# Kernel tuning notes

Measured on AMD Instinct MI355X. Metric: run time of the kernel, lower is better.

Reference implementation:

```python
import jax, jax.numpy as jnp
import numpy as np

ROPE_BASE = 10000.0

def apply_rope(x, offset=0):
    # x: [B, H, L, Dh], traditional (interleaved-pair) RoPE
    B, H, L, Dh = x.shape
    pos = jnp.arange(L, dtype=jnp.float32) + offset            # [L]
    freqs = ROPE_BASE ** (-jnp.arange(0, Dh, 2, dtype=jnp.float32) / Dh)  # [Dh/2]
    theta = pos[:, None] * freqs[None, :]                      # [L, Dh/2]
    cos, sin = jnp.cos(theta), jnp.sin(theta)
    x1 = x[..., 0::2]                                          # [B,H,L,Dh/2]
    x2 = x[..., 1::2]
    r1 = x1 * cos - x2 * sin
    r2 = x1 * sin + x2 * cos
    return jnp.stack([r1, r2], axis=-1).reshape(B, H, L, Dh)


def setup_inputs() -> dict:
    key = jax.random.key(0)
    ks = jax.random.split(key, 5)
    B, L, D = 2, 2048, 2048
    s = 1.0 / np.sqrt(D)
    x = jax.random.normal(ks[0], (B, L, D), dtype=jnp.float32)
    # additive causal mask (0 on/below diagonal, -1e9 above)
    mask = jnp.where(jnp.tril(jnp.ones((L, L), dtype=bool)), 0.0, -1e9).astype(jnp.float32)
    Wq = jax.random.normal(ks[1], (D, D), dtype=jnp.float32) * s
    Wk = jax.random.normal(ks[2], (D, D), dtype=jnp.float32) * s
    Wv = jax.random.normal(ks[3], (D, D), dtype=jnp.float32) * s
    Wo = jax.random.normal(ks[4], (D, D), dtype=jnp.float32) * s
    return {"x": x, "mask": mask, "Wq": Wq, "Wk": Wk, "Wv": Wv, "Wo": Wo}


def reference(x, mask, Wq, Wk, Wv, Wo):
    num_heads = 16
    B, L, D = x.shape
    Dh = D // num_heads
    q = (x @ Wq.T).reshape(B, L, num_heads, Dh).transpose(0, 2, 1, 3)  # [B,H,L,Dh]
    k = (x @ Wk.T).reshape(B, L, num_heads, Dh).transpose(0, 2, 1, 3)
    v = (x @ Wv.T).reshape(B, L, num_heads, Dh).transpose(0, 2, 1, 3)
    q = apply_rope(q)
    k = apply_rope(k)
    scale = 1.0 / jnp.sqrt(jnp.float32(Dh))
    scores = jnp.einsum('bhqd,bhkd->bhqk', q * scale, k) + mask  # [B,H,L,L]
    probs = jax.nn.softmax(scores, axis=-1)
    vh = jnp.einsum('bhqk,bhkd->bhqd', probs, v)                 # [B,H,L,Dh]
    vh = vh.transpose(0, 2, 1, 3).reshape(B, L, D)
    out = vh @ Wo.T
    return out, k, v
```

## Files before the change

kernel.cpp:

```cpp
#include <hip/hip_runtime.h>

typedef __attribute__((ext_vector_type(4))) float f32x4;
typedef __attribute__((ext_vector_type(8))) __bf16 bf16x8;

__device__ __forceinline__ unsigned short f2b(float f) {
  unsigned int u = __builtin_bit_cast(unsigned int, f);
  u = (u + 0x7fffu + ((u >> 16) & 1u)) >> 16;
  return (unsigned short)u;
}
__device__ __forceinline__ float b2f(unsigned short h) {
  unsigned int u = ((unsigned int)h) << 16;
  return __builtin_bit_cast(float, u);
}
__device__ __forceinline__ void gl_lds16(const void* g, void* l) {
  __builtin_amdgcn_global_load_lds(
      (const __attribute__((address_space(1))) void*)g,
      (__attribute__((address_space(3))) void*)l, 16, 0, 0);
}

__global__ void cast_kernel(const float* __restrict__ src,
                            unsigned short* __restrict__ dst, int n4) {
  int i = blockIdx.x * blockDim.x + threadIdx.x;
  if (i >= n4) return;
  float4 v = ((const float4*)src)[i];
  ushort4 o;
  o.x = f2b(v.x); o.y = f2b(v.y); o.z = f2b(v.z); o.w = f2b(v.w);
  ((ushort4*)dst)[i] = o;
}

__global__ void cast4_kernel(const float* __restrict__ s0, const float* __restrict__ s1,
                             const float* __restrict__ s2, const float* __restrict__ s3,
                             unsigned short* __restrict__ d0, unsigned short* __restrict__ d1,
                             unsigned short* __restrict__ d2, unsigned short* __restrict__ d3,
                             int n4) {
  int i = blockIdx.x * blockDim.x + threadIdx.x;
  if (i >= n4) return;
  const float* src = blockIdx.y == 0 ? s0 : blockIdx.y == 1 ? s1 : blockIdx.y == 2 ? s2 : s3;
  unsigned short* dst = blockIdx.y == 0 ? d0 : blockIdx.y == 1 ? d1 : blockIdx.y == 2 ? d2 : d3;
  float4 v = ((const float4*)src)[i];
  ushort4 o;
  o.x = f2b(v.x); o.y = f2b(v.y); o.z = f2b(v.z); o.w = f2b(v.w);
  ((ushort4*)dst)[i] = o;
}

__global__ void rope_table_kernel(float2* __restrict__ tab) {
  int idx = blockIdx.x * blockDim.x + threadIdx.x;
  int l = idx >> 6, i = idx & 63;
  float freq = __builtin_amdgcn_exp2f(-(float)(2 * i) * (13.287712379549449f / 128.0f));
  float th = (float)l * freq;
  tab[idx] = make_float2(cosf(th), sinf(th));
}

__global__ void rope_apply_kernel(unsigned short* __restrict__ qb,
                                  unsigned short* __restrict__ kb,
                                  float* __restrict__ kout,
                                  const float2* __restrict__ tab) {
  const float QS = 0.12751743f;
  int z = blockIdx.y;
  int p = blockIdx.x * blockDim.x + threadIdx.x;
  int i = p & 63;
  int t = p >> 6;
  int h = t & 15; t >>= 4;
  int l = t & 2047;
  int b = t >> 11;
  int base = ((b * 2048 + l) * 2048) + h * 128 + 2 * i;
  unsigned short* buf = z ? kb : qb;
  float x1 = b2f(buf[base]), x2 = b2f(buf[base + 1]);
  float2 cs = tab[l * 64 + i];
  float r1 = x1 * cs.x - x2 * cs.y;
  float r2 = x1 * cs.y + x2 * cs.x;
  if (z == 1) {
    buf[base] = f2b(r1);
    buf[base + 1] = f2b(r2);
    int obase = ((b * 16 + h) * 2048 + l) * 128 + 2 * i;
    kout[obase] = r1; kout[obase + 1] = r2;
  } else {
    buf[base] = f2b(r1 * QS);
    buf[base + 1] = f2b(r2 * QS);
  }
}

__global__ __launch_bounds__(256) void transpose_v_kernel(const unsigned short* __restrict__ vb,
                                                          unsigned short* __restrict__ vt,
                                                          float* __restrict__ vout) {
  __shared__ unsigned short t[32][33];
  int bz = blockIdx.z;
  int b = bz >> 4, h = bz & 15;
  int l0 = blockIdx.x * 32, d0 = blockIdx.y * 32;
  const unsigned short* src = vb + (size_t)b * 2048 * 2048 + h * 128;
  unsigned short* dst = vt + (size_t)bz * 128 * 2048;
  int tx = threadIdx.x & 31, ty = threadIdx.x >> 5;
#pragma unroll
  for (int i = 0; i < 4; ++i) {
    unsigned short u = src[(size_t)(l0 + ty + 8 * i) * 2048 + d0 + tx];
    t[ty + 8 * i][tx] = u;
    vout[((size_t)bz * 2048 + l0 + ty + 8 * i) * 128 + d0 + tx] = b2f(u);
  }
  __syncthreads();
#pragma unroll
  for (int i = 0; i < 4; ++i)
    dst[(size_t)(d0 + ty + 8 * i) * 2048 + l0 + tx] = t[tx][ty + 8 * i];
}

template <int BM, int NBN, int OUT_F32>
__global__ __launch_bounds__(512, 2) void gemm4(const unsigned short* __restrict__ A,
                                                const unsigned short* __restrict__ W,
                                                void* __restrict__ C) {
  constexpr int K = 2048, NT = 32;
  constexpr int AH = BM / 2;
  constexpr int MF = BM / 64;
  constexpr int AQ = AH / 64;
  __shared__ unsigned short Asm[2][2][AH * 64];
  __shared__ unsigned short Bsm[2][2][128 * 64];

  const int tid = threadIdx.x, lane = tid & 63, wv = tid >> 6;
  const int wr = wv >> 2, wc = wv & 3;
  const int ln = lane & 15, kg = lane >> 4;

  const int cpx = (int)gridDim.x >> 3;
  const int swzb = ((int)blockIdx.x & 7) * cpx + ((int)blockIdx.x >> 3);
  const int bm = swzb / NBN, bn = swzb % NBN;
  const int m0 = bm * BM, n0 = bn * 256;

  const int rr = lane >> 3;
  const int sws = ((lane & 7) ^ (rr & 7)) * 8;
  const unsigned short* pA = A + (size_t)(m0 + wv * 8 * AQ + rr) * K + sws;
  const unsigned short* pB = W + (size_t)(n0 + wv * 16 + rr) * K + sws;

#define STA_(dd, hh, tt)                                                         \
  { _Pragma("unroll") for (int q = 0; q < AQ; ++q)                               \
      gl_lds16(pA + ((size_t)(hh)*AH + q * 8) * K + (size_t)(tt)*64,             \
               &Asm[dd][hh][(wv * 8 * AQ + q * 8) * 64 + lane * 8]); }
#define STB_(dd, hh, tt)                                                         \
  { _Pragma("unroll") for (int q = 0; q < 2; ++q)                                \
      gl_lds16(pB + ((size_t)(hh)*128 + q * 8) * K + (size_t)(tt)*64,            \
               &Bsm[dd][hh][(wv * 16 + q * 8) * 64 + lane * 8]); }

  const int sw0 = (kg ^ (ln & 7)) * 8;
  const int sw1 = ((4 + kg) ^ (ln & 7)) * 8;
  const int rae = (wr * (AH / 2) + ln) * 64;
  const int rbe = (wc * 32 + ln) * 64;

  f32x4 acc[2 * MF][4] = {};
  bf16x8 aA[MF][2], bB[2][2][2];

#define LDA_(dd, mh)                                                              \
  { _Pragma("unroll") for (int mf = 0; mf < MF; ++mf) {                           \
      aA[mf][0] = *(const bf16x8*)&Asm[dd][mh][rae + mf * 1024 + sw0];            \
      aA[mf][1] = *(const bf16x8*)&Asm[dd][mh][rae + mf * 1024 + sw1];            \
    } }
#define LDB_(dd, bh)                                                              \
  { _Pragma("unroll") for (int nf = 0; nf < 2; ++nf) {                            \
      bB[bh][nf][0] = *(const bf16x8*)&Bsm[dd][bh][rbe + nf * 1024 + sw0];        \
      bB[bh][nf][1] = *(const bf16x8*)&Bsm[dd][bh][rbe + nf * 1024 + sw1];        \
    } }

#define QMM(mh, bh)                                                               \
  {                                                                               \
    __builtin_amdgcn_s_setprio(1);                                                \
    _Pragma("unroll") for (int mf = 0; mf < MF; ++mf)                             \
        _Pragma("unroll") for (int nf = 0; nf < 2; ++nf) {                        \
      acc[(mh)*MF + mf][(bh)*2 + nf] = __builtin_amdgcn_mfma_f32_16x16x32_bf16(   \
          aA[mf][0], bB[bh][nf][0], acc[(mh)*MF + mf][(bh)*2 + nf], 0, 0, 0);     \
      acc[(mh)*MF + mf][(bh)*2 + nf] = __builtin_amdgcn_mfma_f32_16x16x32_bf16(   \
          aA[mf][1], bB[bh][nf][1], acc[(mh)*MF + mf][(bh)*2 + nf], 0, 0, 0);     \
    }                                                                             \
    __builtin_amdgcn_s_setprio(0);                                                \
  }

#define BAR   { __builtin_amdgcn_s_barrier(); __builtin_amdgcn_sched_barrier(0); }
#define VWAIT                                                                     \
  { if (BM == 256) { asm volatile("s_waitcnt vmcnt(4)" ::: "memory"); }           \
    else { asm volatile("s_waitcnt vmcnt(3)" ::: "memory"); } }
#define VW0   { asm volatile("s_waitcnt vmcnt(0)" ::: "memory"); }

  STA_(0, 0, 0); STB_(0, 0, 0); STB_(0, 1, 0); STA_(0, 1, 0);
  STA_(1, 0, 1); STB_(1, 1, 1);
  VWAIT;

  for (int T = 0; T < NT; T += 2) {
    const bool more = (T + 2) < NT;
    LDA_(0, 0); LDB_(0, 0);
    STB_(1, 0, T + 1);
    BAR; QMM(0, 0); BAR;
    LDB_(0, 1);
    STA_(1, 1, T + 1);
    BAR; QMM(0, 1); BAR;
    LDA_(0, 1);
    if (more) STA_(0, 0, T + 2);
    BAR; QMM(1, 1); BAR;
    if (more) { STB_(0, 1, T + 2); VWAIT; } else { VW0; }
    BAR; QMM(1, 0); BAR;
    LDA_(1, 0); LDB_(1, 0);
    if (more) STB_(0, 0, T + 2);
    BAR; QMM(0, 0); BAR;
    LDB_(1, 1);
    if (more) STA_(0, 1, T + 2);
    BAR; QMM(0, 1); BAR;
    LDA_(1, 1);
    if (more) STA_(1, 0, T + 3);
    BAR; QMM(1, 1); BAR;
    if (more) { STB_(1, 1, T + 3); VWAIT; }
    BAR; QMM(1, 0); BAR;
  }

  const int mat = bn >> 3;
  unsigned short* Cb = (unsigned short*)C;
  float* Cf = (float*)C;
#pragma unroll
  for (int mh = 0; mh < 2; ++mh)
#pragma unroll
    for (int mf = 0; mf < MF; ++mf)
#pragma unroll
      for (int j = 0; j < 4; ++j) {
        int row = m0 + mh * AH + wr * (AH / 2) + mf * 16 + kg * 4 + j;
        size_t rb = (size_t)mat * 8388608 + (size_t)row * 2048 + (size_t)((bn & 7) * 256);
#pragma unroll
        for (int bh = 0; bh < 2; ++bh)
#pragma unroll
          for (int nf = 0; nf < 2; ++nf) {
            int col = bh * 128 + wc * 32 + nf * 16 + ln;
            float v = acc[mh * MF + mf][bh * 2 + nf][j];
            if (OUT_F32) Cf[rb + col] = v;
            else Cb[rb + col] = f2b(v);
          }
      }
#undef STA_
#undef STB_
#undef LDA_
#undef LDB_
#undef QMM
#undef BAR
#undef VWAIT
#undef VW0
}

__global__ __launch_bounds__(256, 2) void attn5_kernel(const unsigned short* __restrict__ Qb,
                                                       const unsigned short* __restrict__ Kb,
                                                       const unsigned short* __restrict__ Vt,
                                                       unsigned short* __restrict__ Ob) {
  __shared__ unsigned short KS[2][8192];
  __shared__ unsigned short VS[8192];
  __shared__ unsigned short PS[4][2048];
  const int D = 2048, L = 2048;
  int tid = threadIdx.x, lane = tid & 63, w = tid >> 6;
  int ln = lane & 15, kg = lane >> 4;
  int bid = blockIdx.x;
  int g = bid >> 5, bh = bid & 31;
  int qt = (g < 8) ? (15 - g) : (g - 8);
  int b = bh >> 4, h = bh & 15;
  const size_t base = (size_t)b * L * D + h * 128;
  const unsigned short* Kp = Kb + base;
  const unsigned short* Qp = Qb + base;
  unsigned short* Op = Ob + base;
  const unsigned short* Vp = Vt + (size_t)bh * 128 * L;

  int q0 = qt * 128;
  int qw0 = q0 + w * 32;

  bf16x8 aq[2][4];
#pragma unroll
  for (int m = 0; m < 2; ++m)
#pragma unroll
    for (int kc = 0; kc < 4; ++kc)
      aq[m][kc] = *(const bf16x8*)&Qp[(size_t)(qw0 + m * 16 + ln) * D + kc * 32 + kg * 8];

  f32x4 o[2][8] = {};
  float m2[2][4], ls[2][4];
#pragma unroll
  for (int m = 0; m < 2; ++m)
#pragma unroll
    for (int j = 0; j < 4; ++j) { m2[m][j] = -1e30f; ls[m][j] = 0.f; }

  int l16 = lane >> 4, l8 = lane >> 3, l7 = lane & 7;

#define STAGE_K(T, NB)                                                                 \
  { int kv0_ = (T) << 6;                                                               \
    _Pragma("unroll") for (int i = 0; i < 4; ++i) {                                    \
      int cK = w * 4 + i;                                                              \
      int r = cK * 4 + l16;                                                            \
      int sw = ln ^ (r & 7);                                                           \
      gl_lds16(Kp + (size_t)(kv0_ + r) * D + sw * 8, &KS[NB][cK * 512 + lane * 8]); } }
#define STAGE_V(T)                                                                     \
  { int kv0_ = (T) << 6;                                                               \
    _Pragma("unroll") for (int i = 0; i < 4; ++i) {                                    \
      int cK = w * 4 + i;                                                              \
      int dh = cK * 8 + l8;                                                            \
      int sv = l7 ^ (dh & 7);                                                          \
      gl_lds16(Vp + (size_t)dh * L + kv0_ + sv * 8, &VS[cK * 512 + lane * 8]); } }

  int nt = 2 * qt + 2;
  int mask_t = 2 * qt + (w >> 1);

  STAGE_K(0, 0);
  __syncthreads();

  for (int t = 0; t < nt; ++t) {
    int cur = t & 1;
    STAGE_V(t);
    bool morek = (t + 1) < nt;
    if (morek) STAGE_K(t + 1, cur ^ 1);

    if (t <= mask_t) {
      int kv0 = t << 6;
      f32x4 s[2][4] = {};
#pragma unroll
      for (int n = 0; n < 4; ++n)
#pragma unroll
        for (int kc = 0; kc < 4; ++kc) {
          bf16x8 bk = *(const bf16x8*)&KS[cur][(n * 16 + ln) * 128 + (((kc << 2) + kg) ^ (ln & 7)) * 8];
          s[0][n] = __builtin_amdgcn_mfma_f32_16x16x32_bf16(aq[0][kc], bk, s[0][n], 0, 0, 0);
          s[1][n] = __builtin_amdgcn_mfma_f32_16x16x32_bf16(aq[1][kc], bk, s[1][n], 0, 0, 0);
        }
      if (t == mask_t) {
#pragma unroll
        for (int m = 0; m < 2; ++m)
#pragma unroll
          for (int n = 0; n < 4; ++n)
#pragma unroll
            for (int j = 0; j < 4; ++j)
              if (kv0 + n * 16 + ln > qw0 + m * 16 + kg * 4 + j) s[m][n][j] = -1e30f;
      }
      float pmax[2][4];
      bool near = true;
#pragma unroll
      for (int m = 0; m < 2; ++m)
#pragma unroll
        for (int j = 0; j < 4; ++j) {
          pmax[m][j] = fmaxf(fmaxf(s[m][0][j], s[m][1][j]), fmaxf(s[m][2][j], s[m][3][j]));
          near = near && (pmax[m][j] <= m2[m][j] + 8.0f);
        }
      if (!__all(near)) {
#pragma unroll
        for (int m = 0; m < 2; ++m)
#pragma unroll
          for (int j = 0; j < 4; ++j) {
            float mx = pmax[m][j];
#pragma unroll
            for (int d = 1; d < 16; d <<= 1) mx = fmaxf(mx, __shfl_xor(mx, d));
            mx = fmaxf(mx, m2[m][j]);
            float al = __builtin_amdgcn_exp2f(m2[m][j] - mx);
            m2[m][j] = mx;
            ls[m][j] *= al;
#pragma unroll
            for (int dt = 0; dt < 8; ++dt) o[m][dt][j] *= al;
          }
      }
#pragma unroll
      for (int m = 0; m < 2; ++m)
#pragma unroll
        for (int j = 0; j < 4; ++j) {
          int row = m * 16 + kg * 4 + j;
          float acc = 0.f;
#pragma unroll
          for (int n = 0; n < 4; ++n) {
            float p = __builtin_amdgcn_exp2f(s[m][n][j] - m2[m][j]);
            acc += p;
            unsigned int u = __builtin_bit_cast(unsigned int, p);
            PS[w][row * 64 + (((n * 2 + (ln >> 3)) ^ (row & 7)) * 8) + (ln & 7)] =
                (unsigned short)(u >> 16);
          }
          ls[m][j] += acc;
        }
    }

    if (morek) { asm volatile("s_waitcnt vmcnt(4)" ::: "memory"); }
    else       { asm volatile("s_waitcnt vmcnt(0)" ::: "memory"); }
    __builtin_amdgcn_s_barrier();
    __builtin_amdgcn_sched_barrier(0);

    if (t <= mask_t) {
      int kv0 = t << 6;
      (void)kv0;
#pragma unroll
      for (int kst = 0; kst < 2; ++kst) {
        bf16x8 ap0 = *(const bf16x8*)&PS[w][(ln) * 64 + (((kst << 2) + kg) ^ (ln & 7)) * 8];
        bf16x8 ap1 = *(const bf16x8*)&PS[w][(16 + ln) * 64 + (((kst << 2) + kg) ^ (ln & 7)) * 8];
#pragma unroll
        for (int dt = 0; dt < 8; ++dt) {
          bf16x8 bv = *(const bf16x8*)&VS[(dt * 16 + ln) * 64 + (((kst << 2) + kg) ^ (ln & 7)) * 8];
          o[0][dt] = __builtin_amdgcn_mfma_f32_16x16x32_bf16(ap0, bv, o[0][dt], 0, 0, 0);
          o[1][dt] = __builtin_amdgcn_mfma_f32_16x16x32_bf16(ap1, bv, o[1][dt], 0, 0, 0);
        }
      }
    }
    __syncthreads();
  }
#undef STAGE_K
#undef STAGE_V

#pragma unroll
  for (int m = 0; m < 2; ++m)
#pragma unroll
    for (int j = 0; j < 4; ++j) {
      float tsum = ls[m][j];
#pragma unroll
      for (int d = 1; d < 16; d <<= 1) tsum += __shfl_xor(tsum, d);
      float inv = 1.0f / tsum;
      int row = qw0 + m * 16 + kg * 4 + j;
#pragma unroll
      for (int dt = 0; dt < 8; ++dt)
        Op[(size_t)row * D + dt * 16 + ln] = f2b(o[m][dt][j] * inv);
    }
}

extern "C" void kernel_launch(void* const* d_in, const int* in_sizes, int n_in,
                              void* d_out, int out_size, void* d_ws, size_t ws_size,
                              hipStream_t stream) {
  const float* x  = (const float*)d_in[0];
  const float* Wq = (const float*)d_in[2];
  const float* Wk = (const float*)d_in[3];
  const float* Wv = (const float*)d_in[4];
  const float* Wo = (const float*)d_in[5];

  char* ws = (char*)d_ws;
  unsigned short* xb  = (unsigned short*)(ws + 0);
  unsigned short* wqb = (unsigned short*)(ws + 16777216);
  unsigned short* wkb = (unsigned short*)(ws + 25165824);
  unsigned short* wvb = (unsigned short*)(ws + 33554432);
  unsigned short* wob = (unsigned short*)(ws + 41943040);
  unsigned short* qb  = (unsigned short*)(ws + 50331648);
  unsigned short* kb  = (unsigned short*)(ws + 67108864);
  unsigned short* vb  = (unsigned short*)(ws + 83886080);
  float2* tab         = (float2*)(ws + 100663296);
  unsigned short* vt  = wqb;
  unsigned short* ob  = xb;

  float* out  = (float*)d_out;
  float* kout = out + 8388608;
  float* vout = out + 16777216;

  cast_kernel<<<8192, 256, 0, stream>>>(x, xb, 2097152);
  cast4_kernel<<<dim3(4096, 4), 256, 0, stream>>>(Wq, Wk, Wv, Wo, wqb, wkb, wvb, wob, 1048576);
  rope_table_kernel<<<512, 256, 0, stream>>>(tab);

  gemm4<256, 24, 0><<<384, 512, 0, stream>>>(xb, wqb, qb);

  transpose_v_kernel<<<dim3(64, 4, 32), 256, 0, stream>>>(vb, vt, vout);

  rope_apply_kernel<<<dim3(16384, 2), 256, 0, stream>>>(qb, kb, kout, tab);

  attn5_kernel<<<512, 256, 0, stream>>>(qb, kb, vt, ob);

  gemm4<128, 8, 1><<<256, 512, 0, stream>>>(ob, wob, out);
}
```

Before: 296.4 us.

## Merge prep and post-projection kernels, add MFMA priority hints in attention

The three cast/rope-table kernels are folded into one launch with a blockIdx.y selector, and the V transpose and RoPE apply kernels are folded into a second launch. This removes launch overhead and the gaps between small kernels. The attention kernel also raises wave priority with s_setprio around the MFMA loops so matrix work is issued ahead of other waves. The merged grids leave many idle blocks that exit early, and the transpose branch adds LDS use to the RoPE path, which may affect occupancy.

```diff
diff --git a/kernel.cpp b/kernel.cpp
--- a/kernel.cpp
+++ b/kernel.cpp
@@ -18,9 +18,28 @@
       (__attribute__((address_space(3))) void*)l, 16, 0, 0);
 }
 
-__global__ void cast_kernel(const float* __restrict__ src,
-                            unsigned short* __restrict__ dst, int n4) {
+__global__ void prep_kernel(const float* __restrict__ x, unsigned short* __restrict__ xb,
+                            const float* __restrict__ s0, const float* __restrict__ s1,
+                            const float* __restrict__ s2, const float* __restrict__ s3,
+                            unsigned short* __restrict__ d0, unsigned short* __restrict__ d1,
+                            unsigned short* __restrict__ d2, unsigned short* __restrict__ d3,
+                            float2* __restrict__ tab) {
+  int z = blockIdx.y;
   int i = blockIdx.x * blockDim.x + threadIdx.x;
+  if (z == 5) {
+    if (i >= 131072) return;
+    int l = i >> 6, k = i & 63;
+    float freq = __builtin_amdgcn_exp2f(-(float)(2 * k) * (13.287712379549449f / 128.0f));
+    float th = (float)l * freq;
+    tab[i] = make_float2(cosf(th), sinf(th));
+    return;
+  }
+  const float* src; unsigned short* dst; int n4;
+  if (z == 0)      { src = x;  dst = xb; n4 = 2097152; }
+  else if (z == 1) { src = s0; dst = d0; n4 = 1048576; }
+  else if (z == 2) { src = s1; dst = d1; n4 = 1048576; }
+  else if (z == 3) { src = s2; dst = d2; n4 = 1048576; }
+  else             { src = s3; dst = d3; n4 = 1048576; }
   if (i >= n4) return;
   float4 v = ((const float4*)src)[i];
   ushort4 o;
@@ -28,41 +47,43 @@
   ((ushort4*)dst)[i] = o;
 }
 
-__global__ void cast4_kernel(const float* __restrict__ s0, const float* __restrict__ s1,
-                             const float* __restrict__ s2, const float* __restrict__ s3,
-                             unsigned short* __restrict__ d0, unsigned short* __restrict__ d1,
-                             unsigned short* __restrict__ d2, unsigned short* __restrict__ d3,
-                             int n4) {
-  int i = blockIdx.x * blockDim.x + threadIdx.x;
-  if (i >= n4) return;
-  const float* src = blockIdx.y == 0 ? s0 : blockIdx.y == 1 ? s1 : blockIdx.y == 2 ? s2 : s3;
-  unsigned short* dst = blockIdx.y == 0 ? d0 : blockIdx.y == 1 ? d1 : blockIdx.y == 2 ? d2 : d3;
-  float4 v = ((const float4*)src)[i];
-  ushort4 o;
-  o.x = f2b(v.x); o.y = f2b(v.y); o.z = f2b(v.z); o.w = f2b(v.w);
-  ((ushort4*)dst)[i] = o;
-}
-
-__global__ void rope_table_kernel(float2* __restrict__ tab) {
-  int idx = blockIdx.x * blockDim.x + threadIdx.x;
-  int l = idx >> 6, i = idx & 63;
-  float freq = __builtin_amdgcn_exp2f(-(float)(2 * i) * (13.287712379549449f / 128.0f));
-  float th = (float)l * freq;
-  tab[idx] = make_float2(cosf(th), sinf(th));
-}
-
-__global__ void rope_apply_kernel(unsigned short* __restrict__ qb,
-                                  unsigned short* __restrict__ kb,
-                                  float* __restrict__ kout,
-                                  const float2* __restrict__ tab) {
+__global__ __launch_bounds__(256) void fix_kernel(unsigned short* __restrict__ qb,
+                                                  unsigned short* __restrict__ kb,
+                                                  float* __restrict__ kout,
+                                                  const unsigned short* __restrict__ vb,
+                                                  unsigned short* __restrict__ vt,
+                                                  float* __restrict__ vout,
+                                                  const float2* __restrict__ tab) {
+  __shared__ unsigned short t[32][33];
   const float QS = 0.12751743f;
   int z = blockIdx.y;
+  if (z == 2) {
+    int bid = blockIdx.x;
+    if (bid >= 8192) return;
+    int lx = bid & 63, dy = (bid >> 6) & 3, bz = bid >> 8;
+    int b = bz >> 4, h = bz & 15;
+    int l0 = lx * 32, d0 = dy * 32;
+    const unsigned short* src = vb + (size_t)b * 2048 * 2048 + h * 128;
+    unsigned short* dst = vt + (size_t)bz * 128 * 2048;
+    int tx = threadIdx.x & 31, ty = threadIdx.x >> 5;
+#pragma unroll
+    for (int i = 0; i < 4; ++i) {
+      unsigned short u = src[(size_t)(l0 + ty + 8 * i) * 2048 + d0 + tx];
+      t[ty + 8 * i][tx] = u;
+      vout[((size_t)bz * 2048 + l0 + ty + 8 * i) * 128 + d0 + tx] = b2f(u);
+    }
+    __syncthreads();
+#pragma unroll
+    for (int i = 0; i < 4; ++i)
+      dst[(size_t)(d0 + ty + 8 * i) * 2048 + l0 + tx] = t[tx][ty + 8 * i];
+    return;
+  }
   int p = blockIdx.x * blockDim.x + threadIdx.x;
   int i = p & 63;
-  int t = p >> 6;
-  int h = t & 15; t >>= 4;
-  int l = t & 2047;
-  int b = t >> 11;
+  int tt = p >> 6;
+  int h = tt & 15; tt >>= 4;
+  int l = tt & 2047;
+  int b = tt >> 11;
   int base = ((b * 2048 + l) * 2048) + h * 128 + 2 * i;
   unsigned short* buf = z ? kb : qb;
   float x1 = b2f(buf[base]), x2 = b2f(buf[base + 1]);
@@ -78,28 +99,6 @@
     buf[base] = f2b(r1 * QS);
     buf[base + 1] = f2b(r2 * QS);
   }
-}
-
-__global__ __launch_bounds__(256) void transpose_v_kernel(const unsigned short* __restrict__ vb,
-                                                          unsigned short* __restrict__ vt,
-                                                          float* __restrict__ vout) {
-  __shared__ unsigned short t[32][33];
-  int bz = blockIdx.z;
-  int b = bz >> 4, h = bz & 15;
-  int l0 = blockIdx.x * 32, d0 = blockIdx.y * 32;
-  const unsigned short* src = vb + (size_t)b * 2048 * 2048 + h * 128;
-  unsigned short* dst = vt + (size_t)bz * 128 * 2048;
-  int tx = threadIdx.x & 31, ty = threadIdx.x >> 5;
-#pragma unroll
-  for (int i = 0; i < 4; ++i) {
-    unsigned short u = src[(size_t)(l0 + ty + 8 * i) * 2048 + d0 + tx];
-    t[ty + 8 * i][tx] = u;
-    vout[((size_t)bz * 2048 + l0 + ty + 8 * i) * 128 + d0 + tx] = b2f(u);
-  }
-  __syncthreads();
-#pragma unroll
-  for (int i = 0; i < 4; ++i)
-    dst[(size_t)(d0 + ty + 8 * i) * 2048 + l0 + tx] = t[tx][ty + 8 * i];
 }
 
 template <int BM, int NBN, int OUT_F32>
@@ -304,6 +303,7 @@
     if (t <= mask_t) {
       int kv0 = t << 6;
       f32x4 s[2][4] = {};
+      __builtin_amdgcn_s_setprio(1);
 #pragma unroll
       for (int n = 0; n < 4; ++n)
 #pragma unroll
@@ -312,6 +312,7 @@
           s[0][n] = __builtin_amdgcn_mfma_f32_16x16x32_bf16(aq[0][kc], bk, s[0][n], 0, 0, 0);
           s[1][n] = __builtin_amdgcn_mfma_f32_16x16x32_bf16(aq[1][kc], bk, s[1][n], 0, 0, 0);
         }
+      __builtin_amdgcn_s_setprio(0);
       if (t == mask_t) {
 #pragma unroll
         for (int m = 0; m < 2; ++m)
@@ -370,8 +371,7 @@
     __builtin_amdgcn_sched_barrier(0);
 
     if (t <= mask_t) {
-      int kv0 = t << 6;
-      (void)kv0;
+      __builtin_amdgcn_s_setprio(1);
 #pragma unroll
       for (int kst = 0; kst < 2; ++kst) {
         bf16x8 ap0 = *(const bf16x8*)&PS[w][(ln) * 64 + (((kst << 2) + kg) ^ (ln & 7)) * 8];
@@ -383,6 +383,7 @@
           o[1][dt] = __builtin_amdgcn_mfma_f32_16x16x32_bf16(ap1, bv, o[1][dt], 0, 0, 0);
         }
       }
+      __builtin_amdgcn_s_setprio(0);
     }
     __syncthreads();
   }
@@ -430,15 +431,11 @@
   float* kout = out + 8388608;
   float* vout = out + 16777216;
 
-  cast_kernel<<<8192, 256, 0, stream>>>(x, xb, 2097152);
-  cast4_kernel<<<dim3(4096, 4), 256, 0, stream>>>(Wq, Wk, Wv, Wo, wqb, wkb, wvb, wob, 1048576);
-  rope_table_kernel<<<512, 256, 0, stream>>>(tab);
+  prep_kernel<<<dim3(8192, 6), 256, 0, stream>>>(x, xb, Wq, Wk, Wv, Wo, wqb, wkb, wvb, wob, tab);
 
   gemm4<256, 24, 0><<<384, 512, 0, stream>>>(xb, wqb, qb);
 
-  transpose_v_kernel<<<dim3(64, 4, 32), 256, 0, stream>>>(vb, vt, vout);
-
-  rope_apply_kernel<<<dim3(16384, 2), 256, 0, stream>>>(qb, kb, kout, tab);
+  fix_kernel<<<dim3(16384, 3), 256, 0, stream>>>(qb, kb, kout, vb, vt, vout, tab);
 
   attn5_kernel<<<512, 256, 0, stream>>>(qb, kb, vt, ob);
 
```

Result: no change. 294.8 us (median of 2 runs) (-0.6%).
